# Optimization experiments

Hardware: AMD Instinct MI355X
Metric: run time of the kernel (lower is better)

Reference implementation:

```python
import jax, jax.numpy as jnp
import numpy as np


def setup_inputs() -> dict:
    key = jax.random.key(0)
    k1, k2, k3 = jax.random.split(key, 3)
    seq_len, input_size, hidden_size = 8192, 2048, 2048
    inputs = jax.random.normal(k1, (seq_len, input_size), dtype=jnp.float32)
    W_xh = jax.random.normal(k2, (hidden_size, input_size), dtype=jnp.float32) * 0.01
    W_hh = jax.random.normal(k3, (hidden_size, hidden_size), dtype=jnp.float32) * 0.01
    b_h = jnp.zeros((hidden_size, 1), dtype=jnp.float32)
    return {"inputs": inputs, "W_xh": W_xh, "W_hh": W_hh, "b_h": b_h}


def reference(inputs, W_xh, W_hh, b_h):
    # h_t = tanh(W_xh @ x_t + W_hh @ h_{t-1} + b_h), h_0 = 0
    # Torch code uses column vectors (hidden,1); we use flat (hidden,) vectors,
    # which is the same math.
    b = b_h[:, 0]
    h0 = jnp.zeros((W_hh.shape[0],), dtype=inputs.dtype)

    def step(h_prev, x_t):
        h_t = jnp.tanh(W_xh @ x_t + W_hh @ h_prev + b)
        return h_t, h_t

    h_T, outputs = jax.lax.scan(step, h0, inputs)
    # outputs: (seq_len, hidden)  == stacked list of h_t; h_T == final state
    return outputs, h_T
```

## Files before the change

kernel.cpp:

```cpp
#include <hip/hip_runtime.h>
#include <math.h>

#define H 2048
#define S 8192
#define RPB 8
#define NBLK (H / RPB)
#define PW16 (H / 4)
#define NREP 2

typedef float f32x4 __attribute__((ext_vector_type(4)));
typedef unsigned int u32x4 __attribute__((ext_vector_type(4)));

__global__ __launch_bounds__(256) void gemm_xw(const float* __restrict__ X,
                                               const float* __restrict__ W,
                                               float* __restrict__ U) {
    __shared__ float As[16][64];
    __shared__ float Bs[16][64];
    const int tid = threadIdx.x;
    const int t0 = blockIdx.x * 64;
    const int j0 = blockIdx.y * 64;
    const int tx = tid & 15, ty = tid >> 4;

    float acc[4][4] = {};
    const int lr = tid >> 2;
    const int lk = (tid & 3) * 4;

    for (int k0 = 0; k0 < H; k0 += 16) {
        float4 a = *(const float4*)&X[(size_t)(t0 + lr) * H + k0 + lk];
        float4 b = *(const float4*)&W[(size_t)(j0 + lr) * H + k0 + lk];
        As[lk + 0][lr] = a.x; As[lk + 1][lr] = a.y; As[lk + 2][lr] = a.z; As[lk + 3][lr] = a.w;
        Bs[lk + 0][lr] = b.x; Bs[lk + 1][lr] = b.y; Bs[lk + 2][lr] = b.z; Bs[lk + 3][lr] = b.w;
        __syncthreads();
#pragma unroll
        for (int kk = 0; kk < 16; ++kk) {
            float4 av = *(const float4*)&As[kk][ty * 4];
            float4 bv = *(const float4*)&Bs[kk][tx * 4];
            float aa[4] = {av.x, av.y, av.z, av.w};
            float bb[4] = {bv.x, bv.y, bv.z, bv.w};
#pragma unroll
            for (int i = 0; i < 4; ++i)
#pragma unroll
                for (int j = 0; j < 4; ++j)
                    acc[i][j] += aa[i] * bb[j];
        }
        __syncthreads();
    }
#pragma unroll
    for (int i = 0; i < 4; ++i) {
        float4 v = {acc[i][0], acc[i][1], acc[i][2], acc[i][3]};
        *(float4*)&U[(size_t)(t0 + ty * 4 + i) * H + j0 + tx * 4] = v;
    }
}

__global__ void init_ws(unsigned int* __restrict__ w) {
    int i = blockIdx.x * blockDim.x + threadIdx.x;
    if (i < NREP * 2 * PW16 * 4) w[i] = (i >> 11) & 1u;
}

__device__ inline u32x4 ld16_sc1(const void* p) {
    u32x4 r;
    asm volatile("global_load_dwordx4 %0, %1, off sc1\n\t"
                 "s_waitcnt vmcnt(0)"
                 : "=&v"(r) : "v"(p) : "memory");
    return r;
}
__device__ inline void ld16x2_sc1(const void* p0, const void* p1, u32x4& a, u32x4& b) {
    asm volatile("global_load_dwordx4 %0, %2, off sc1\n\t"
                 "global_load_dwordx4 %1, %3, off sc1\n\t"
                 "s_waitcnt vmcnt(0)"
                 : "=&v"(a), "=&v"(b) : "v"(p0), "v"(p1) : "memory");
}
__device__ inline void st16_sc1(void* p, u32x4 v) {
    asm volatile("global_store_dwordx4 %0, %1, off sc1" :: "v"(p), "v"(v) : "memory");
}

__global__ __launch_bounds__(256) void rnn_recur(float* __restrict__ out,
                                                 const float* __restrict__ Whh,
                                                 const float* __restrict__ bias,
                                                 unsigned long long* __restrict__ hvt) {
    __shared__ __align__(16) float red[2][RPB][4];
    const int tid = threadIdx.x;
    const int r0 = blockIdx.x * RPB;
    const int lane = tid & 63;
    const int wid = tid >> 6;

    float4 wv[RPB][2];
#pragma unroll
    for (int j = 0; j < RPB; ++j)
#pragma unroll
        for (int i = 0; i < 2; ++i)
            wv[j][i] = *(const float4*)&Whh[(size_t)(r0 + j) * H + 4 * (i * 256 + tid)];

    const float bb = bias[r0 + (tid & 7)];
    f32x4* const hbase = (f32x4*)hvt;
    int fb = 0;

    for (int t = 0; t < S; ++t) {
        float u_val = out[(size_t)t * H + r0 + (tid & 7)];

        const unsigned int ep = ((unsigned int)t >> 1) & 1u;
        const f32x4* hb = hbase + (size_t)(blockIdx.x & 1) * (2 * PW16) +
                          (size_t)(t & 1) * PW16;
        float acc[RPB] = {};
        unsigned int pend = 3u;
        int spin = 0;

        while (pend && !fb) {
            u32x4 va, vb;
            if (pend == 3u)      ld16x2_sc1(hb + tid, hb + 256 + tid, va, vb);
            else if (pend == 1u) va = ld16_sc1(hb + tid);
            else                 vb = ld16_sc1(hb + 256 + tid);
            if (pend & 1u) {
                if ((((va.x ^ ep) | (va.y ^ ep) | (va.z ^ ep) | (va.w ^ ep)) & 1u) == 0u) {
                    const float h0 = __uint_as_float(va.x), h1 = __uint_as_float(va.y);
                    const float h2 = __uint_as_float(va.z), h3 = __uint_as_float(va.w);
#pragma unroll
                    for (int j = 0; j < RPB; ++j)
                        acc[j] += wv[j][0].x * h0 + wv[j][0].y * h1 +
                                  wv[j][0].z * h2 + wv[j][0].w * h3;
                    pend &= ~1u;
                }
            }
            if (pend & 2u) {
                if ((((vb.x ^ ep) | (vb.y ^ ep) | (vb.z ^ ep) | (vb.w ^ ep)) & 1u) == 0u) {
                    const float h0 = __uint_as_float(vb.x), h1 = __uint_as_float(vb.y);
                    const float h2 = __uint_as_float(vb.z), h3 = __uint_as_float(vb.w);
#pragma unroll
                    for (int j = 0; j < RPB; ++j)
                        acc[j] += wv[j][1].x * h0 + wv[j][1].y * h1 +
                                  wv[j][1].z * h2 + wv[j][1].w * h3;
                    pend &= ~2u;
                }
            }
            if (pend) {
                __builtin_amdgcn_s_sleep(1);
                if (++spin > 512) fb = 1;
            }
        }
        while (pend) {
#pragma unroll
            for (int i = 0; i < 2; ++i)
                if (pend & (1u << i)) {
                    const unsigned long long* q =
                        (const unsigned long long*)(hb + i * 256 + tid);
                    unsigned long long lo = __hip_atomic_load(q, __ATOMIC_RELAXED,
                                                              __HIP_MEMORY_SCOPE_AGENT);
                    unsigned long long hi = __hip_atomic_load(q + 1, __ATOMIC_RELAXED,
                                                              __HIP_MEMORY_SCOPE_AGENT);
                    u32x4 v; v.x = (unsigned int)lo; v.y = (unsigned int)(lo >> 32);
                    v.z = (unsigned int)hi; v.w = (unsigned int)(hi >> 32);
                    if ((((v.x ^ ep) | (v.y ^ ep) | (v.z ^ ep) | (v.w ^ ep)) & 1u) == 0u) {
                        const float h0 = __uint_as_float(v.x), h1 = __uint_as_float(v.y);
                        const float h2 = __uint_as_float(v.z), h3 = __uint_as_float(v.w);
#pragma unroll
                        for (int j = 0; j < RPB; ++j)
                            acc[j] += wv[j][i].x * h0 + wv[j][i].y * h1 +
                                      wv[j][i].z * h2 + wv[j][i].w * h3;
                        pend &= ~(1u << i);
                    }
                }
            if (pend) __builtin_amdgcn_s_sleep(1);
        }

#pragma unroll
        for (int j = 0; j < 4; ++j) {
            float s = (lane & 1) ? acc[j] : acc[j + 4];
            float r = __shfl_xor(s, 1, 64);
            acc[j] = ((lane & 1) ? acc[j + 4] : acc[j]) + r;
        }
#pragma unroll
        for (int j = 0; j < 2; ++j) {
            float s = (lane & 2) ? acc[j] : acc[j + 2];
            float r = __shfl_xor(s, 2, 64);
            acc[j] = ((lane & 2) ? acc[j + 2] : acc[j]) + r;
        }
        {
            float s = (lane & 4) ? acc[0] : acc[1];
            float r = __shfl_xor(s, 4, 64);
            acc[0] = ((lane & 4) ? acc[1] : acc[0]) + r;
        }
#pragma unroll
        for (int m = 8; m <= 32; m <<= 1)
            acc[0] += __shfl_xor(acc[0], m, 64);
        if (lane < 8)
            red[t & 1][((lane & 1) << 2) | (lane & 2) | ((lane & 4) >> 2)][wid] = acc[0];
        __syncthreads();

        if (tid < 8) {
            const float4 r4 = *(const float4*)red[t & 1][tid];
            const float val = tanhf(r4.x + r4.y + r4.z + r4.w + u_val + bb);
            out[(size_t)t * H + r0 + tid] = val;
            if (t == S - 1) out[(size_t)S * H + r0 + tid] = val;
            const float p0 = __shfl(val, (int)(tid & 4) | 0, 64);
            const float p1 = __shfl(val, (int)(tid & 4) | 1, 64);
            const float p2 = __shfl(val, (int)(tid & 4) | 2, 64);
            const float p3 = __shfl(val, (int)(tid & 4) | 3, 64);
            if ((tid & 3) == 0) {
                const unsigned int e2 = (((unsigned int)(t + 1)) >> 1) & 1u;
                u32x4 pk;
                pk.x = (__float_as_uint(p0) & ~1u) | e2;
                pk.y = (__float_as_uint(p1) & ~1u) | e2;
                pk.z = (__float_as_uint(p2) & ~1u) | e2;
                pk.w = (__float_as_uint(p3) & ~1u) | e2;
                const int widx = (r0 >> 2) + (tid >> 2);
                const size_t par = (size_t)((t + 1) & 1) * PW16;
#pragma unroll
                for (int rep = 0; rep < NREP; ++rep)
                    st16_sc1(hbase + (size_t)rep * (2 * PW16) + par + widx, pk);
            }
        }
    }
}

extern "C" void kernel_launch(void* const* d_in, const int* in_sizes, int n_in,
                              void* d_out, int out_size, void* d_ws, size_t ws_size,
                              hipStream_t stream) {
    const float* X    = (const float*)d_in[0];
    const float* Wxh  = (const float*)d_in[1];
    const float* Whh  = (const float*)d_in[2];
    const float* bias = (const float*)d_in[3];
    float* out = (float*)d_out;
    unsigned long long* hvt = (unsigned long long*)d_ws;

    init_ws<<<(NREP * 2 * PW16 * 4 + 255) / 256, 256, 0, stream>>>((unsigned int*)hvt);

    dim3 ggrid(S / 64, H / 64);
    gemm_xw<<<ggrid, 256, 0, stream>>>(X, Wxh, out);

    void* args[] = {(void*)&out, (void*)&Whh, (void*)&bias, (void*)&hvt};
    hipLaunchCooperativeKernel((void*)rnn_recur, dim3(NBLK), dim3(256), args, 0, stream);
}
```

Before: 23.76 ms.

## Prefetch next-step hidden chunks while polling and replace block barrier with flags

The persistent recurrence kernel now polls both the current and the next parity buffer in each spin iteration. Any next-step hidden chunks that have already arrived are accumulated into a second accumulator set, so part of step t+1's matvec overlaps the wait for step t. The __syncthreads reduction is replaced by per-wave LDS flags that only wave 0 spins on, and each thread's W_hh slice now covers 8 contiguous columns so it can read 32 contiguous bytes. The trade-off is extra polling loads per spin and more register pressure, and the atomic-load fallback now kicks in only after many more spins.

Result: slower. 28.80 ms (+21.2%).

```diff
diff --git a/kernel.cpp b/kernel.cpp
--- a/kernel.cpp
+++ b/kernel.cpp
@@ -5,10 +5,9 @@
 #define S 8192
 #define RPB 8
 #define NBLK (H / RPB)
-#define PW16 (H / 4)
+#define PARBYTES (H * 4)
 #define NREP 2
 
-typedef float f32x4 __attribute__((ext_vector_type(4)));
 typedef unsigned int u32x4 __attribute__((ext_vector_type(4)));
 
 __global__ __launch_bounds__(256) void gemm_xw(const float* __restrict__ X,
@@ -52,23 +51,23 @@
     }
 }
 
-__global__ void init_ws(unsigned int* __restrict__ w) {
+__global__ void init_ws(unsigned long long* __restrict__ w) {
     int i = blockIdx.x * blockDim.x + threadIdx.x;
-    if (i < NREP * 2 * PW16 * 4) w[i] = (i >> 11) & 1u;
-}
-
-__device__ inline u32x4 ld16_sc1(const void* p) {
-    u32x4 r;
-    asm volatile("global_load_dwordx4 %0, %1, off sc1\n\t"
-                 "s_waitcnt vmcnt(0)"
-                 : "=&v"(r) : "v"(p) : "memory");
-    return r;
-}
-__device__ inline void ld16x2_sc1(const void* p0, const void* p1, u32x4& a, u32x4& b) {
-    asm volatile("global_load_dwordx4 %0, %2, off sc1\n\t"
-                 "global_load_dwordx4 %1, %3, off sc1\n\t"
-                 "s_waitcnt vmcnt(0)"
-                 : "=&v"(a), "=&v"(b) : "v"(p0), "v"(p1) : "memory");
+    if (i < NREP * 2 * (PARBYTES / 8))
+        w[i] = ((i >> 10) & 1) ? 0x0000000100000001ull : 0ull;
+}
+
+__device__ inline void poll4(const void* pc, const void* pn,
+                             u32x4& c0, u32x4& c1, u32x4& n0, u32x4& n1) {
+    asm volatile(
+        "global_load_dwordx4 %0, %4, off sc1\n\t"
+        "global_load_dwordx4 %1, %4, off offset:16 sc1\n\t"
+        "global_load_dwordx4 %2, %5, off sc1\n\t"
+        "global_load_dwordx4 %3, %5, off offset:16 sc1\n\t"
+        "s_waitcnt vmcnt(0)"
+        : "=&v"(c0), "=&v"(c1), "=&v"(n0), "=&v"(n1)
+        : "v"(pc), "v"(pn)
+        : "memory");
 }
 __device__ inline void st16_sc1(void* p, u32x4 v) {
     asm volatile("global_store_dwordx4 %0, %1, off sc1" :: "v"(p), "v"(v) : "memory");
@@ -78,77 +77,57 @@
                                                  const float* __restrict__ Whh,
                                                  const float* __restrict__ bias,
                                                  unsigned long long* __restrict__ hvt) {
-    __shared__ __align__(16) float red[2][RPB][4];
-    const int tid = threadIdx.x;
-    const int r0 = blockIdx.x * RPB;
+    __shared__ float part[2][4][RPB];
+    __shared__ int   flag[2][4];
+    const int tid  = threadIdx.x;
     const int lane = tid & 63;
-    const int wid = tid >> 6;
+    const int wid  = tid >> 6;
+    const int r0   = blockIdx.x * RPB;
+
+    if (tid < 8) flag[tid >> 2][tid & 3] = 0;
+    __syncthreads();
 
     float4 wv[RPB][2];
 #pragma unroll
     for (int j = 0; j < RPB; ++j)
 #pragma unroll
         for (int i = 0; i < 2; ++i)
-            wv[j][i] = *(const float4*)&Whh[(size_t)(r0 + j) * H + 4 * (i * 256 + tid)];
+            wv[j][i] = *(const float4*)&Whh[(size_t)(r0 + j) * H + 8 * tid + 4 * i];
 
     const float bb = bias[r0 + (tid & 7)];
-    f32x4* const hbase = (f32x4*)hvt;
-    int fb = 0;
+    char* const hrep = (char*)hvt + (size_t)(blockIdx.x & 1) * (2 * PARBYTES);
+
+    float acc[RPB] = {}, accN[RPB] = {};
+    unsigned int pend = 3u, pendN = 3u;
 
     for (int t = 0; t < S; ++t) {
         float u_val = out[(size_t)t * H + r0 + (tid & 7)];
 
-        const unsigned int ep = ((unsigned int)t >> 1) & 1u;
-        const f32x4* hb = hbase + (size_t)(blockIdx.x & 1) * (2 * PW16) +
-                          (size_t)(t & 1) * PW16;
-        float acc[RPB] = {};
-        unsigned int pend = 3u;
+        const unsigned int ep  = ((unsigned int)t >> 1) & 1u;
+        const unsigned int epN = ((unsigned int)(t + 1) >> 1) & 1u;
+        const char* pc = hrep + (size_t)(t & 1) * PARBYTES + tid * 32;
+        const char* pn = hrep + (size_t)((t + 1) & 1) * PARBYTES + tid * 32;
+
         int spin = 0;
-
-        while (pend && !fb) {
-            u32x4 va, vb;
-            if (pend == 3u)      ld16x2_sc1(hb + tid, hb + 256 + tid, va, vb);
-            else if (pend == 1u) va = ld16_sc1(hb + tid);
-            else                 vb = ld16_sc1(hb + 256 + tid);
-            if (pend & 1u) {
-                if ((((va.x ^ ep) | (va.y ^ ep) | (va.z ^ ep) | (va.w ^ ep)) & 1u) == 0u) {
-                    const float h0 = __uint_as_float(va.x), h1 = __uint_as_float(va.y);
-                    const float h2 = __uint_as_float(va.z), h3 = __uint_as_float(va.w);
-#pragma unroll
-                    for (int j = 0; j < RPB; ++j)
-                        acc[j] += wv[j][0].x * h0 + wv[j][0].y * h1 +
-                                  wv[j][0].z * h2 + wv[j][0].w * h3;
-                    pend &= ~1u;
+        while (pend) {
+            u32x4 c[2], n[2];
+            poll4(pc, pn, c[0], c[1], n[0], n[1]);
+            if (__builtin_expect(spin > 4096, 0)) {
+                const unsigned long long* q = (const unsigned long long*)pc;
+#pragma unroll
+                for (int i = 0; i < 2; ++i) {
+                    unsigned long long lo = __hip_atomic_load(q + 2 * i, __ATOMIC_RELAXED,
+                                                              __HIP_MEMORY_SCOPE_AGENT);
+                    unsigned long long hi = __hip_atomic_load(q + 2 * i + 1, __ATOMIC_RELAXED,
+                                                              __HIP_MEMORY_SCOPE_AGENT);
+                    c[i].x = (unsigned int)lo; c[i].y = (unsigned int)(lo >> 32);
+                    c[i].z = (unsigned int)hi; c[i].w = (unsigned int)(hi >> 32);
                 }
             }
-            if (pend & 2u) {
-                if ((((vb.x ^ ep) | (vb.y ^ ep) | (vb.z ^ ep) | (vb.w ^ ep)) & 1u) == 0u) {
-                    const float h0 = __uint_as_float(vb.x), h1 = __uint_as_float(vb.y);
-                    const float h2 = __uint_as_float(vb.z), h3 = __uint_as_float(vb.w);
-#pragma unroll
-                    for (int j = 0; j < RPB; ++j)
-                        acc[j] += wv[j][1].x * h0 + wv[j][1].y * h1 +
-                                  wv[j][1].z * h2 + wv[j][1].w * h3;
-                    pend &= ~2u;
-                }
-            }
-            if (pend) {
-                __builtin_amdgcn_s_sleep(1);
-                if (++spin > 512) fb = 1;
-            }
-        }
-        while (pend) {
-#pragma unroll
-            for (int i = 0; i < 2; ++i)
+#pragma unroll
+            for (int i = 0; i < 2; ++i) {
                 if (pend & (1u << i)) {
-                    const unsigned long long* q =
-                        (const unsigned long long*)(hb + i * 256 + tid);
-                    unsigned long long lo = __hip_atomic_load(q, __ATOMIC_RELAXED,
-                                                              __HIP_MEMORY_SCOPE_AGENT);
-                    unsigned long long hi = __hip_atomic_load(q + 1, __ATOMIC_RELAXED,
-                                                              __HIP_MEMORY_SCOPE_AGENT);
-                    u32x4 v; v.x = (unsigned int)lo; v.y = (unsigned int)(lo >> 32);
-                    v.z = (unsigned int)hi; v.w = (unsigned int)(hi >> 32);
+                    const u32x4 v = c[i];
                     if ((((v.x ^ ep) | (v.y ^ ep) | (v.z ^ ep) | (v.w ^ ep)) & 1u) == 0u) {
                         const float h0 = __uint_as_float(v.x), h1 = __uint_as_float(v.y);
                         const float h2 = __uint_as_float(v.z), h3 = __uint_as_float(v.w);
@@ -159,7 +138,23 @@
                         pend &= ~(1u << i);
                     }
                 }
-            if (pend) __builtin_amdgcn_s_sleep(1);
+                if (pendN & (1u << i)) {
+                    const u32x4 v = n[i];
+                    if ((((v.x ^ epN) | (v.y ^ epN) | (v.z ^ epN) | (v.w ^ epN)) & 1u) == 0u) {
+                        const float h0 = __uint_as_float(v.x), h1 = __uint_as_float(v.y);
+                        const float h2 = __uint_as_float(v.z), h3 = __uint_as_float(v.w);
+#pragma unroll
+                        for (int j = 0; j < RPB; ++j)
+                            accN[j] += wv[j][i].x * h0 + wv[j][i].y * h1 +
+                                       wv[j][i].z * h2 + wv[j][i].w * h3;
+                        pendN &= ~(1u << i);
+                    }
+                }
+            }
+            if (pend) {
+                __builtin_amdgcn_s_sleep(1);
+                ++spin;
+            }
         }
 
 #pragma unroll
@@ -182,33 +177,50 @@
 #pragma unroll
         for (int m = 8; m <= 32; m <<= 1)
             acc[0] += __shfl_xor(acc[0], m, 64);
+
         if (lane < 8)
-            red[t & 1][((lane & 1) << 2) | (lane & 2) | ((lane & 4) >> 2)][wid] = acc[0];
-        __syncthreads();
-
-        if (tid < 8) {
-            const float4 r4 = *(const float4*)red[t & 1][tid];
-            const float val = tanhf(r4.x + r4.y + r4.z + r4.w + u_val + bb);
-            out[(size_t)t * H + r0 + tid] = val;
-            if (t == S - 1) out[(size_t)S * H + r0 + tid] = val;
-            const float p0 = __shfl(val, (int)(tid & 4) | 0, 64);
-            const float p1 = __shfl(val, (int)(tid & 4) | 1, 64);
-            const float p2 = __shfl(val, (int)(tid & 4) | 2, 64);
-            const float p3 = __shfl(val, (int)(tid & 4) | 3, 64);
-            if ((tid & 3) == 0) {
+            part[t & 1][wid][((lane & 1) << 2) | (lane & 2) | ((lane & 4) >> 2)] = acc[0];
+        __threadfence_block();
+        if (lane == 0)
+            __hip_atomic_store(&flag[t & 1][wid], t + 1, __ATOMIC_RELEASE,
+                               __HIP_MEMORY_SCOPE_WORKGROUP);
+
+        if (wid == 0 && lane < 8) {
+            while (__hip_atomic_load(&flag[t & 1][0], __ATOMIC_ACQUIRE,
+                                     __HIP_MEMORY_SCOPE_WORKGROUP) < t + 1 ||
+                   __hip_atomic_load(&flag[t & 1][1], __ATOMIC_ACQUIRE,
+                                     __HIP_MEMORY_SCOPE_WORKGROUP) < t + 1 ||
+                   __hip_atomic_load(&flag[t & 1][2], __ATOMIC_ACQUIRE,
+                                     __HIP_MEMORY_SCOPE_WORKGROUP) < t + 1 ||
+                   __hip_atomic_load(&flag[t & 1][3], __ATOMIC_ACQUIRE,
+                                     __HIP_MEMORY_SCOPE_WORKGROUP) < t + 1) { }
+            const float sum = part[t & 1][0][lane] + part[t & 1][1][lane] +
+                              part[t & 1][2][lane] + part[t & 1][3][lane];
+            const float val = tanhf(sum + u_val + bb);
+            out[(size_t)t * H + r0 + lane] = val;
+            if (t == S - 1) out[(size_t)S * H + r0 + lane] = val;
+            const float s0 = __shfl(val, (lane & 4) | 0, 64);
+            const float s1 = __shfl(val, (lane & 4) | 1, 64);
+            const float s2 = __shfl(val, (lane & 4) | 2, 64);
+            const float s3 = __shfl(val, (lane & 4) | 3, 64);
+            if ((lane & 3) == 0) {
                 const unsigned int e2 = (((unsigned int)(t + 1)) >> 1) & 1u;
                 u32x4 pk;
-                pk.x = (__float_as_uint(p0) & ~1u) | e2;
-                pk.y = (__float_as_uint(p1) & ~1u) | e2;
-                pk.z = (__float_as_uint(p2) & ~1u) | e2;
-                pk.w = (__float_as_uint(p3) & ~1u) | e2;
-                const int widx = (r0 >> 2) + (tid >> 2);
-                const size_t par = (size_t)((t + 1) & 1) * PW16;
+                pk.x = (__float_as_uint(s0) & ~1u) | e2;
+                pk.y = (__float_as_uint(s1) & ~1u) | e2;
+                pk.z = (__float_as_uint(s2) & ~1u) | e2;
+                pk.w = (__float_as_uint(s3) & ~1u) | e2;
+                char* dst = (char*)hvt + (size_t)((t + 1) & 1) * PARBYTES +
+                            (size_t)r0 * 4 + (lane & 4) * 4;
 #pragma unroll
                 for (int rep = 0; rep < NREP; ++rep)
-                    st16_sc1(hbase + (size_t)rep * (2 * PW16) + par + widx, pk);
-            }
-        }
+                    st16_sc1(dst + (size_t)rep * (2 * PARBYTES), pk);
+            }
+        }
+
+#pragma unroll
+        for (int j = 0; j < RPB; ++j) { acc[j] = accN[j]; accN[j] = 0.f; }
+        pend = pendN; pendN = 3u;
     }
 }
 
@@ -222,7 +234,7 @@
     float* out = (float*)d_out;
     unsigned long long* hvt = (unsigned long long*)d_ws;
 
-    init_ws<<<(NREP * 2 * PW16 * 4 + 255) / 256, 256, 0, stream>>>((unsigned int*)hvt);
+    init_ws<<<(NREP * 2 * (PARBYTES / 8) + 255) / 256, 256, 0, stream>>>(hvt);
 
     dim3 ggrid(S / 64, H / 64);
     gemm_xw<<<ggrid, 256, 0, stream>>>(X, Wxh, out);
```
